# Performance work log

Hardware: AMD Instinct MI355X
Metric: run time of the kernel (lower is better)

Reference implementation:

```python
import jax, jax.numpy as jnp
import numpy as np

GRID = (8, 8)
EPS = 1e-5  # nn.BatchNorm2d default eps


def _per_tile(t, g, b, w, cb):
    # t: (B, C, th, tw); training-mode BatchNorm over (B, th, tw) per channel
    mean = t.mean(axis=(0, 2, 3))
    var = t.var(axis=(0, 2, 3))  # biased variance, matches torch BN normalization
    xn = (t - mean[:, None, None]) * jax.lax.rsqrt(var[:, None, None] + EPS)
    h = jax.nn.relu(xn * g[:, None, None] + b[:, None, None])
    y = jax.lax.conv_general_dilated(
        h, w, window_strides=(1, 1), padding='SAME',
        dimension_numbers=('NCHW', 'OIHW', 'NCHW'))
    return y + cb[:, None, None] + t  # conv bias + residual


def setup_inputs() -> dict:
    key = jax.random.key(0)
    k1, k2 = jax.random.split(key)
    B, C, H, W = 32, 32, 160, 160
    n_tiles = GRID[0] * GRID[1]
    x = jax.random.normal(k1, (B, C, H, W), dtype=jnp.float32)
    gamma = jnp.ones((n_tiles, C), dtype=jnp.float32)
    beta = jnp.zeros((n_tiles, C), dtype=jnp.float32)
    # kaiming-ish init for 3x3 conv
    conv_w = jax.random.normal(k2, (n_tiles, C, C, 3, 3), dtype=jnp.float32) * (2.0 / (C * 9)) ** 0.5
    conv_b = jnp.zeros((n_tiles, C), dtype=jnp.float32)
    return {"x": x, "gamma": gamma, "beta": beta, "conv_w": conv_w, "conv_b": conv_b}


def reference(x, gamma, beta, conv_w, conv_b):
    B, C, H, W = x.shape
    gi, gj = GRID
    th, tw = H // gi, W // gj
    # split into (gi*gj, B, C, th, tw) tiles
    tiles = x.reshape(B, C, gi, th, gj, tw).transpose(2, 4, 0, 1, 3, 5)
    tiles = tiles.reshape(gi * gj, B, C, th, tw)
    out = jax.vmap(_per_tile)(tiles, gamma, beta, conv_w, conv_b)
    # reassemble
    out = out.reshape(gi, gj, B, C, th, tw).transpose(2, 3, 0, 4, 1, 5)
    return out.reshape(B, C, H, W)
```

## Files before the change

kernel.cpp:

```cpp
#include <hip/hip_runtime.h>

#define NT 64
#define B_ 32
#define C_ 32
#define H_ 160
#define W_ 160
#define TH 20
#define TW 20
#define NPIX (TH*TW)
#define NRED (B_*NPIX)
#define EPS 1e-5f

#define HP 40
#define WSL 33

typedef __bf16 bf16x8 __attribute__((ext_vector_type(8)));
typedef float  f32x4  __attribute__((ext_vector_type(4)));

__global__ __launch_bounds__(320) void statsA_kernel(const float* __restrict__ x,
                                                     float* __restrict__ ppS,
                                                     float* __restrict__ ppS2) {
    int blk = blockIdx.x;
    int b = blk >> 5;
    int c = blk & 31;
    const float* plane = x + ((long)(b*C_ + c)) * H_ * W_;

    int tid   = threadIdx.x;
    int col4  = tid % 40;
    int rbase = tid / 40;

    __shared__ float sh [8 * 321];
    __shared__ float sh2[8 * 321];

    #pragma unroll
    for (int tr = 0; tr < 8; ++tr) {
        float s = 0.f, s2 = 0.f;
        #pragma unroll
        for (int k = 0; k < 3; ++k) {
            int r20 = rbase + 8*k;
            if (r20 < 20) {
                int row = tr*20 + r20;
                float4 v = *(const float4*)(plane + row*W_ + col4*4);
                s  += v.x + v.y + v.z + v.w;
                s2 += v.x*v.x + v.y*v.y + v.z*v.z + v.w*v.w;
            }
        }
        sh [tr*321 + tid] = s;
        sh2[tr*321 + tid] = s2;
    }
    __syncthreads();

    if (tid < 64) {
        int tr = tid >> 3, tc = tid & 7;
        float ps = 0.f, ps2 = 0.f;
        #pragma unroll
        for (int rb = 0; rb < 8; ++rb)
            #pragma unroll
            for (int c5 = 0; c5 < 5; ++c5) {
                int t = tr*321 + rb*40 + tc*5 + c5;
                ps += sh[t]; ps2 += sh2[t];
            }
        int tl = tr*8 + tc;
        atomicAdd(&ppS [tl*C_ + c], ps);
        atomicAdd(&ppS2[tl*C_ + c], ps2);
    }
}

__global__ __launch_bounds__(512, 4) void fused_kernel(
        const float* __restrict__ x,
        const float* __restrict__ gamma,
        const float* __restrict__ beta,
        const float* __restrict__ conv_w,
        const float* __restrict__ conv_b,
        const float* __restrict__ ppS,
        const float* __restrict__ ppS2,
        float* __restrict__ out) {
    int blk = blockIdx.x;
    int tl = blk >> 5;
    int b  = blk & 31;
    int ti = (tl >> 3) * TH;
    int tj = (tl & 7)  * TW;
    int tid = threadIdx.x;

    __shared__ __align__(16) unsigned char smem[62656];
    __bf16* hlds   = (__bf16*)smem;
    __bf16* wlds   = (__bf16*)(smem + 38720);
    float*  scale  = (float*)(smem + 62400);
    float*  shiftv = (float*)(smem + 62528);

    if (tid < 420) {
        int hp = tid / 5, q = tid - hp*5;
        int P;
        if      (hp < 22) P = hp;
        else if (hp < 44) P = 462 + (hp - 22);
        else if (hp < 64) P = (hp - 43) * 22;
        else              P = (hp - 63) * 22 + 21;
        ((uint4*)smem)[P*5 + q] = uint4{0,0,0,0};
    }
    if (tid < C_) {
        int c = tid;
        float s   = ppS [tl*C_ + c];
        float s2  = ppS2[tl*C_ + c];
        float m   = s / (float)NRED;
        float var = s2 / (float)NRED - m*m;
        float rs  = rsqrtf(var + EPS);
        float g   = gamma[tl*C_ + c];
        scale[c]  = g * rs;
        shiftv[c] = beta[tl*C_ + c] - m * rs * g;
    }
    {
        const float* wsrc = conv_w + (long)tl * (C_*C_*9);
        for (int f = tid; f < C_*C_*9; f += 512) {
            int co  = f / 288;
            int rem = f - co*288;
            int cin = rem / 9;
            int tap = rem - cin*9;
            wlds[(tap*WSL + co)*HP + cin] = (__bf16)wsrc[f];
        }
    }
    __syncthreads();

    for (int idx = tid; idx < 4*NPIX; idx += 512) {
        int cg = idx / NPIX;
        int p  = idx - cg*NPIX;
        int y  = p / 20;
        int xx = p - y*20;
        int c0 = cg*8;
        const float* ps = x + (((long)(b*C_ + c0)*H_ + ti + y)*W_ + tj + xx);
        float v[8];
        #pragma unroll
        for (int k = 0; k < 8; ++k) v[k] = ps[k * (H_*W_)];
        bf16x8 h;
        #pragma unroll
        for (int k = 0; k < 8; ++k)
            h[k] = (__bf16)fmaxf(v[k]*scale[c0+k] + shiftv[c0+k], 0.f);
        *(bf16x8*)&hlds[((y+1)*22 + xx + 1)*HP + c0] = h;
    }
    __syncthreads();

    int lane = tid & 63;
    int wv   = tid >> 6;
    int mm   = lane & 15;
    int jg   = lane >> 4;
    int j0   = jg * 8;
    float b0 = conv_b[tl*C_ + mm];
    float b1 = conv_b[tl*C_ + 16 + mm];

    auto store_chunk = [&](int chunk, f32x4 a0, f32x4 a1) {
        int pb = chunk*16 + jg*4;
        int py = pb / 20;
        int px = pb - py*20;
        long o0 = ((long)(b*C_ + mm)*H_ + ti + py)*W_ + tj + px;
        long o1 = o0 + (long)16*H_*W_;
        float4 x0 = *(const float4*)&x[o0];
        float4 x1 = *(const float4*)&x[o1];
        float4 r0 = make_float4(a0[0]+x0.x, a0[1]+x0.y, a0[2]+x0.z, a0[3]+x0.w);
        float4 r1 = make_float4(a1[0]+x1.x, a1[1]+x1.y, a1[2]+x1.z, a1[3]+x1.w);
        *(float4*)&out[o0] = r0;
        *(float4*)&out[o1] = r1;
    };

    const __bf16* ab[3];
    #pragma unroll
    for (int i = 0; i < 3; ++i) {
        int p  = (wv + 8*i)*16 + mm;
        int py = p / 20;
        int px = p - py*20;
        ab[i] = &hlds[(py*22 + px)*HP + j0];
    }
    f32x4 acc[3][2];
    #pragma unroll
    for (int i = 0; i < 3; ++i) {
        acc[i][0] = f32x4{b0,b0,b0,b0};
        acc[i][1] = f32x4{b1,b1,b1,b1};
    }
    #pragma unroll
    for (int tap = 0; tap < 9; ++tap) {
        const int ky = tap/3, kx = tap - (tap/3)*3;
        bf16x8 w0 = *(const bf16x8*)&wlds[(tap*WSL + mm)*HP + j0];
        bf16x8 w1 = *(const bf16x8*)&wlds[(tap*WSL + 16 + mm)*HP + j0];
        #pragma unroll
        for (int i = 0; i < 3; ++i) {
            bf16x8 af = *(const bf16x8*)(ab[i] + (ky*22 + kx)*HP);
            acc[i][0] = __builtin_amdgcn_mfma_f32_16x16x32_bf16(af, w0, acc[i][0], 0, 0, 0);
            acc[i][1] = __builtin_amdgcn_mfma_f32_16x16x32_bf16(af, w1, acc[i][1], 0, 0, 0);
        }
    }
    #pragma unroll
    for (int i = 0; i < 3; ++i) store_chunk(wv + 8*i, acc[i][0], acc[i][1]);

    if (wv == 0) {
        int p  = 24*16 + mm;
        int py = p / 20;
        int px = p - py*20;
        const __bf16* a3 = &hlds[(py*22 + px)*HP + j0];
        f32x4 c0v = f32x4{b0,b0,b0,b0};
        f32x4 c1v = f32x4{b1,b1,b1,b1};
        #pragma unroll
        for (int tap = 0; tap < 9; ++tap) {
            const int ky = tap/3, kx = tap - (tap/3)*3;
            bf16x8 w0 = *(const bf16x8*)&wlds[(tap*WSL + mm)*HP + j0];
            bf16x8 w1 = *(const bf16x8*)&wlds[(tap*WSL + 16 + mm)*HP + j0];
            bf16x8 af = *(const bf16x8*)(a3 + (ky*22 + kx)*HP);
            c0v = __builtin_amdgcn_mfma_f32_16x16x32_bf16(af, w0, c0v, 0, 0, 0);
            c1v = __builtin_amdgcn_mfma_f32_16x16x32_bf16(af, w1, c1v, 0, 0, 0);
        }
        store_chunk(24, c0v, c1v);
    }
}

extern "C" void kernel_launch(void* const* d_in, const int* in_sizes, int n_in,
                              void* d_out, int out_size, void* d_ws, size_t ws_size,
                              hipStream_t stream) {
    const float* x      = (const float*)d_in[0];
    const float* gamma  = (const float*)d_in[1];
    const float* beta   = (const float*)d_in[2];
    const float* conv_w = (const float*)d_in[3];
    const float* conv_b = (const float*)d_in[4];
    float* out = (float*)d_out;

    float* ppS  = (float*)d_ws;
    float* ppS2 = ppS + NT*C_;

    hipMemsetAsync(d_ws, 0, 2 * NT * C_ * sizeof(float), stream);
    statsA_kernel<<<B_ * C_, 320, 0, stream>>>(x, ppS, ppS2);
    fused_kernel<<<NT * B_, 512, 0, stream>>>(x, gamma, beta, conv_w, conv_b,
                                              ppS, ppS2, out);
}
```

Measured before the change: 271.5 us.

## Prepack bf16 conv weights once in stats kernel and read them from global

```diff
diff --git a/kernel.cpp b/kernel.cpp
--- a/kernel.cpp
+++ b/kernel.cpp
@@ -13,14 +13,36 @@
 
 #define HP 40
 #define WSL 33
+#define WPACK_PER_TILE (9*2*64*8)
 
 typedef __bf16 bf16x8 __attribute__((ext_vector_type(8)));
 typedef float  f32x4  __attribute__((ext_vector_type(4)));
 
 __global__ __launch_bounds__(320) void statsA_kernel(const float* __restrict__ x,
                                                      float* __restrict__ ppS,
-                                                     float* __restrict__ ppS2) {
+                                                     float* __restrict__ ppS2,
+                                                     const float* __restrict__ conv_w,
+                                                     __bf16* __restrict__ wpack) {
     int blk = blockIdx.x;
+    if (blk >= B_*C_) {
+        int tl = blk - B_*C_;
+        const float* wsrc = conv_w + (long)tl * (C_*C_*9);
+        __bf16* wdst = wpack + (long)tl * WPACK_PER_TILE;
+        for (int f = threadIdx.x; f < WPACK_PER_TILE; f += 320) {
+            int t    = f >> 10;
+            int r    = f & 1023;
+            int h    = r >> 9;
+            int r2   = r & 511;
+            int lane = r2 >> 3;
+            int k    = r2 & 7;
+            int mm   = lane & 15;
+            int jg   = lane >> 4;
+            int co   = h*16 + mm;
+            int cin  = jg*8 + k;
+            wdst[f] = (__bf16)wsrc[(co*C_ + cin)*9 + t];
+        }
+        return;
+    }
     int b = blk >> 5;
     int c = blk & 31;
     const float* plane = x + ((long)(b*C_ + c)) * H_ * W_;
@@ -66,7 +88,140 @@
     }
 }
 
-__global__ __launch_bounds__(512, 4) void fused_kernel(
+__global__ __launch_bounds__(512, 8) void fused_packed(
+        const float* __restrict__ x,
+        const float* __restrict__ gamma,
+        const float* __restrict__ beta,
+        const float* __restrict__ conv_b,
+        const float* __restrict__ ppS,
+        const float* __restrict__ ppS2,
+        const __bf16* __restrict__ wpack,
+        float* __restrict__ out) {
+    int blk = blockIdx.x;
+    int tl = blk >> 5;
+    int b  = blk & 31;
+    int ti = (tl >> 3) * TH;
+    int tj = (tl & 7)  * TW;
+    int tid = threadIdx.x;
+
+    __shared__ __align__(16) unsigned char smem[38976];
+    __bf16* hlds   = (__bf16*)smem;
+    float*  scale  = (float*)(smem + 38720);
+    float*  shiftv = (float*)(smem + 38848);
+
+    if (tid < 420) {
+        int hp = tid / 5, q = tid - hp*5;
+        int P;
+        if      (hp < 22) P = hp;
+        else if (hp < 44) P = 462 + (hp - 22);
+        else if (hp < 64) P = (hp - 43) * 22;
+        else              P = (hp - 63) * 22 + 21;
+        ((uint4*)smem)[P*5 + q] = uint4{0,0,0,0};
+    }
+    if (tid < C_) {
+        int c = tid;
+        float s   = ppS [tl*C_ + c];
+        float s2  = ppS2[tl*C_ + c];
+        float m   = s / (float)NRED;
+        float var = s2 / (float)NRED - m*m;
+        float rs  = rsqrtf(var + EPS);
+        float g   = gamma[tl*C_ + c];
+        scale[c]  = g * rs;
+        shiftv[c] = beta[tl*C_ + c] - m * rs * g;
+    }
+    __syncthreads();
+
+    for (int idx = tid; idx < 4*NPIX; idx += 512) {
+        int cg = idx / NPIX;
+        int p  = idx - cg*NPIX;
+        int y  = p / 20;
+        int xx = p - y*20;
+        int c0 = cg*8;
+        const float* ps = x + (((long)(b*C_ + c0)*H_ + ti + y)*W_ + tj + xx);
+        float v[8];
+        #pragma unroll
+        for (int k = 0; k < 8; ++k) v[k] = ps[k * (H_*W_)];
+        bf16x8 h;
+        #pragma unroll
+        for (int k = 0; k < 8; ++k)
+            h[k] = (__bf16)fmaxf(v[k]*scale[c0+k] + shiftv[c0+k], 0.f);
+        *(bf16x8*)&hlds[((y+1)*22 + xx + 1)*HP + c0] = h;
+    }
+    __syncthreads();
+
+    int lane = tid & 63;
+    int wv   = tid >> 6;
+    int mm   = lane & 15;
+    int jg   = lane >> 4;
+    int j0   = jg * 8;
+    float b0 = conv_b[tl*C_ + mm];
+    float b1 = conv_b[tl*C_ + 16 + mm];
+    const __bf16* wp = wpack + (long)tl * WPACK_PER_TILE + lane*8;
+
+    auto store_chunk = [&](int chunk, f32x4 a0, f32x4 a1) {
+        int pb = chunk*16 + jg*4;
+        int py = pb / 20;
+        int px = pb - py*20;
+        long o0 = ((long)(b*C_ + mm)*H_ + ti + py)*W_ + tj + px;
+        long o1 = o0 + (long)16*H_*W_;
+        float4 x0 = *(const float4*)&x[o0];
+        float4 x1 = *(const float4*)&x[o1];
+        float4 r0 = make_float4(a0[0]+x0.x, a0[1]+x0.y, a0[2]+x0.z, a0[3]+x0.w);
+        float4 r1 = make_float4(a1[0]+x1.x, a1[1]+x1.y, a1[2]+x1.z, a1[3]+x1.w);
+        *(float4*)&out[o0] = r0;
+        *(float4*)&out[o1] = r1;
+    };
+
+    const __bf16* ab[3];
+    #pragma unroll
+    for (int i = 0; i < 3; ++i) {
+        int p  = (wv + 8*i)*16 + mm;
+        int py = p / 20;
+        int px = p - py*20;
+        ab[i] = &hlds[(py*22 + px)*HP + j0];
+    }
+    f32x4 acc[3][2];
+    #pragma unroll
+    for (int i = 0; i < 3; ++i) {
+        acc[i][0] = f32x4{b0,b0,b0,b0};
+        acc[i][1] = f32x4{b1,b1,b1,b1};
+    }
+    #pragma unroll
+    for (int tap = 0; tap < 9; ++tap) {
+        const int ky = tap/3, kx = tap - (tap/3)*3;
+        bf16x8 w0 = *(const bf16x8*)(wp + tap*1024);
+        bf16x8 w1 = *(const bf16x8*)(wp + tap*1024 + 512);
+        #pragma unroll
+        for (int i = 0; i < 3; ++i) {
+            bf16x8 af = *(const bf16x8*)(ab[i] + (ky*22 + kx)*HP);
+            acc[i][0] = __builtin_amdgcn_mfma_f32_16x16x32_bf16(af, w0, acc[i][0], 0, 0, 0);
+            acc[i][1] = __builtin_amdgcn_mfma_f32_16x16x32_bf16(af, w1, acc[i][1], 0, 0, 0);
+        }
+    }
+    #pragma unroll
+    for (int i = 0; i < 3; ++i) store_chunk(wv + 8*i, acc[i][0], acc[i][1]);
+
+    if (wv == 0) {
+        int p  = 24*16 + mm;
+        int py = p / 20;
+        int px = p - py*20;
+        const __bf16* a3 = &hlds[(py*22 + px)*HP + j0];
+        f32x4 c0v = f32x4{b0,b0,b0,b0};
+        f32x4 c1v = f32x4{b1,b1,b1,b1};
+        #pragma unroll
+        for (int tap = 0; tap < 9; ++tap) {
+            const int ky = tap/3, kx = tap - (tap/3)*3;
+            bf16x8 w0 = *(const bf16x8*)(wp + tap*1024);
+            bf16x8 w1 = *(const bf16x8*)(wp + tap*1024 + 512);
+            bf16x8 af = *(const bf16x8*)(a3 + (ky*22 + kx)*HP);
+            c0v = __builtin_amdgcn_mfma_f32_16x16x32_bf16(af, w0, c0v, 0, 0, 0);
+            c1v = __builtin_amdgcn_mfma_f32_16x16x32_bf16(af, w1, c1v, 0, 0, 0);
+        }
+        store_chunk(24, c0v, c1v);
+    }
+}
+
+__global__ __launch_bounds__(512, 4) void fused_lds(
         const float* __restrict__ x,
         const float* __restrict__ gamma,
         const float* __restrict__ beta,
@@ -219,11 +374,20 @@
     const float* conv_b = (const float*)d_in[4];
     float* out = (float*)d_out;
 
-    float* ppS  = (float*)d_ws;
-    float* ppS2 = ppS + NT*C_;
-
-    hipMemsetAsync(d_ws, 0, 2 * NT * C_ * sizeof(float), stream);
-    statsA_kernel<<<B_ * C_, 320, 0, stream>>>(x, ppS, ppS2);
-    fused_kernel<<<NT * B_, 512, 0, stream>>>(x, gamma, beta, conv_w, conv_b,
-                                              ppS, ppS2, out);
+    float*  ppS   = (float*)d_ws;
+    float*  ppS2  = ppS + NT*C_;
+    size_t  statsBytes = (size_t)2 * NT * C_ * sizeof(float);
+    __bf16* wpack = (__bf16*)((char*)d_ws + statsBytes);
+    size_t  need  = statsBytes + (size_t)NT * WPACK_PER_TILE * sizeof(__bf16);
+
+    hipMemsetAsync(d_ws, 0, statsBytes, stream);
+    if (ws_size >= need) {
+        statsA_kernel<<<B_*C_ + NT, 320, 0, stream>>>(x, ppS, ppS2, conv_w, wpack);
+        fused_packed<<<NT * B_, 512, 0, stream>>>(x, gamma, beta, conv_b,
+                                                  ppS, ppS2, wpack, out);
+    } else {
+        statsA_kernel<<<B_*C_, 320, 0, stream>>>(x, ppS, ppS2, conv_w, wpack);
+        fused_lds<<<NT * B_, 512, 0, stream>>>(x, gamma, beta, conv_w, conv_b,
+                                               ppS, ppS2, out);
+    }
 }
```

New measurement: 295.2 us. 1.09x slower.
